# Kernel optimization log

Hardware: AMD Instinct MI355X
Metric: run time of the kernel (lower is better)

Reference implementation:

```python
import jax, jax.numpy as jnp
import numpy as np
from jax import lax

N, D, H, E = 8192, 1024, 4096, 8


def setup_inputs() -> dict:
    key = jax.random.key(0)
    ks = jax.random.split(key, 4)
    return {
        "x": jax.random.normal(ks[0], (N, D), dtype=jnp.float32),
        "wg": jax.random.normal(ks[1], (D, E), dtype=jnp.float32) * 0.001,
        "fc1_w": jax.random.normal(ks[2], (E, D, H), dtype=jnp.float32) * 0.001,
        "fc1_b": jnp.zeros((E, 1, H), dtype=jnp.float32),
        "fc2_w": jax.random.normal(ks[3], (E, H, D), dtype=jnp.float32) * 0.001,
        "fc2_b": jnp.zeros((E, 1, D), dtype=jnp.float32),
        "k": 2,
    }


def reference(x, wg, fc1_w, fc1_b, fc2_w, fc2_b, k):
    n, d = x.shape
    e = wg.shape[1]
    cap = (k * n) // e  # expert capacity (capacity factor 1.0)

    # --- gate ---
    scores = jax.nn.softmax(x @ wg, axis=-1)          # [N,E]
    topv, topi = lax.top_k(scores, k)                 # [N,k]

    # --- top-k routing: position of each (token, slot) within its expert buffer ---
    masks = jax.nn.one_hot(topi, e, dtype=jnp.int32)  # [N,k,E]
    # slot-major priority: all slot-0 assignments before slot-1
    m = jnp.transpose(masks, (1, 0, 2)).reshape(k * n, e)
    pos_flat = jnp.cumsum(m, axis=0) - m              # position before own assignment
    pos = jnp.sum(pos_flat * m, axis=1).reshape(k, n).T   # [N,k]
    valid = pos < cap                                  # capacity overflow -> dropped

    # --- load-balance aux loss (top-1 fraction * mean gate prob) ---
    me = scores.mean(axis=0)                           # [E]
    ce = masks[:, 0, :].astype(scores.dtype).mean(axis=0)
    l_aux = e * jnp.sum(me * ce)

    # --- encode (dispatch): scatter tokens into [E, C, D] buffers ---
    w = valid.astype(x.dtype)                          # [N,k]
    flat_idx = topi * cap + jnp.where(valid, pos, 0)   # [N,k]
    contrib = (x[:, None, :] * w[:, :, None]).reshape(-1, d)
    dispatched = jnp.zeros((e * cap, d), x.dtype).at[flat_idx.reshape(-1)].add(contrib)
    dispatched = dispatched.reshape(e, cap, d)

    # --- batched expert FFN (all-to-all is identity on one device) ---
    h = jax.nn.relu(jnp.einsum('ecd,edh->ech', dispatched, fc1_w) + fc1_b)
    y = jnp.einsum('ech,ehd->ecd', h, fc2_w) + fc2_b   # [E,C,D]

    # --- decode (combine): gather back and weight by gate scores ---
    gathered = y.reshape(e * cap, d)[flat_idx]         # [N,k,D]
    output = jnp.einsum('nk,nkd->nd', topv * w, gathered)
    return output, l_aux
```

## Files before the change

### kernel.cpp

```cpp
#include <hip/hip_runtime.h>
#include <hip/hip_bf16.h>
#include <stdint.h>

#define N_TOK 8192
#define DMODEL 1024
#define HDIM 4096
#define NEXP 8
#define CAP 2048
#define GATE_BLOCKS (N_TOK / 4)

typedef float floatx4 __attribute__((ext_vector_type(4)));
typedef int int32x4_t __attribute__((ext_vector_type(4)));
typedef int int32x8_t __attribute__((ext_vector_type(8)));

static __device__ __forceinline__ void async_copy16(const void* g, void* l) {
  __builtin_amdgcn_global_load_lds(
      (const __attribute__((address_space(1))) void*)g,
      (__attribute__((address_space(3))) void*)l, 16, 0, 0);
}

static __device__ __forceinline__ unsigned int pk4_fp8(float a, float b, float c, float d) {
  int r = __builtin_amdgcn_cvt_pk_fp8_f32(a, b, 0, 0);
  r = __builtin_amdgcn_cvt_pk_fp8_f32(c, d, r, 1);
  return (unsigned int)r;
}

static __device__ __forceinline__ unsigned short f2bf(float f) {
  union { float f; uint32_t u; } v; v.f = f;
  uint32_t r = (v.u + 0x7FFFu + ((v.u >> 16) & 1u)) >> 16;
  return (unsigned short)r;
}

static __device__ __forceinline__ float bf2f(unsigned short u) {
  union { float f; uint32_t u32; } v; v.u32 = ((uint32_t)u) << 16;
  return v.f;
}

__global__ __launch_bounds__(256) void gate_kernel(
    const float* __restrict__ x, const float* __restrict__ wg,
    float* __restrict__ topv, int* __restrict__ topi,
    float* __restrict__ me_part, int* __restrict__ ce_part) {
  __shared__ float sm_p[4][NEXP];
  __shared__ int sm_i0[4];
  int wave = threadIdx.x >> 6;
  int lane = threadIdx.x & 63;
  int n = blockIdx.x * 4 + wave;
  float acc[NEXP];
#pragma unroll
  for (int e = 0; e < NEXP; e++) acc[e] = 0.f;
  const float* xr = x + (size_t)n * DMODEL;
#pragma unroll 4
  for (int i = 0; i < DMODEL / 64; i++) {
    int idx = lane + 64 * i;
    float xv = xr[idx];
    const float4* wr = (const float4*)(wg + (size_t)idx * NEXP);
    float4 w0 = wr[0], w1 = wr[1];
    acc[0] += xv * w0.x; acc[1] += xv * w0.y;
    acc[2] += xv * w0.z; acc[3] += xv * w0.w;
    acc[4] += xv * w1.x; acc[5] += xv * w1.y;
    acc[6] += xv * w1.z; acc[7] += xv * w1.w;
  }
#pragma unroll
  for (int e = 0; e < NEXP; e++) {
    float v = acc[e];
#pragma unroll
    for (int off = 32; off > 0; off >>= 1) v += __shfl_down(v, off, 64);
    acc[e] = v;
  }
  if (lane == 0) {
    float mx = acc[0];
#pragma unroll
    for (int e = 1; e < NEXP; e++) mx = fmaxf(mx, acc[e]);
    float p[NEXP]; float s = 0.f;
#pragma unroll
    for (int e = 0; e < NEXP; e++) { p[e] = expf(acc[e] - mx); s += p[e]; }
    float inv = 1.f / s;
#pragma unroll
    for (int e = 0; e < NEXP; e++) p[e] *= inv;
    int i0 = 0; float v0 = p[0];
#pragma unroll
    for (int e = 1; e < NEXP; e++) if (p[e] > v0) { v0 = p[e]; i0 = e; }
    int i1 = -1; float v1 = -1.f;
#pragma unroll
    for (int e = 0; e < NEXP; e++) {
      if (e == i0) continue;
      if (p[e] > v1) { v1 = p[e]; i1 = e; }
    }
    topv[n * 2] = v0; topv[n * 2 + 1] = v1;
    topi[n * 2] = i0; topi[n * 2 + 1] = i1;
#pragma unroll
    for (int e = 0; e < NEXP; e++) sm_p[wave][e] = p[e];
    sm_i0[wave] = i0;
  }
  __syncthreads();
  if (threadIdx.x < NEXP) {
    int e = threadIdx.x;
    float pm = 0.f; int cc = 0;
#pragma unroll
    for (int w = 0; w < 4; w++) {
      pm += sm_p[w][e];
      cc += (sm_i0[w] == e) ? 1 : 0;
    }
    me_part[blockIdx.x * NEXP + e] = pm;
    ce_part[blockIdx.x * NEXP + e] = cc;
  }
}

__global__ __launch_bounds__(1024) void scan_kernel(
    const int* __restrict__ topi, const float* __restrict__ topv,
    int* __restrict__ flat_idx, float* __restrict__ cw) {
  __shared__ int hist[16][NEXP];
  __shared__ int base[NEXP];
  int tid = threadIdx.x;
  int w = tid >> 6, lane = tid & 63;
  if (tid < NEXP) base[tid] = 0;
  int vals[16];
#pragma unroll
  for (int c = 0; c < 16; c++) {
    int j = c * 1024 + tid;
    vals[c] = topi[(size_t)(j & 8191) * 2 + (j >> 13)];
  }
  __syncthreads();
  for (int c = 0; c < 16; c++) {
    int j = c * 1024 + tid;
    int slot = j >> 13;
    int n = j & 8191;
    int e = vals[c];
    int rank = 0;
#pragma unroll
    for (int ee = 0; ee < NEXP; ee++) {
      unsigned long long m = __ballot(e == ee);
      if (e == ee) rank = __popcll(m & ((1ull << lane) - 1ull));
      if (lane == ee) hist[w][ee] = __popcll(m);
    }
    __syncthreads();
    if (tid < NEXP) {
      int run = base[tid];
#pragma unroll
      for (int ww = 0; ww < 16; ww++) {
        int t = hist[ww][tid];
        hist[ww][tid] = run;
        run += t;
      }
      base[tid] = run;
    }
    __syncthreads();
    int pos = hist[w][e] + rank;
    bool valid = pos < CAP;
    flat_idx[n * 2 + slot] = e * CAP + (valid ? pos : 0);
    cw[n * 2 + slot] = valid ? topv[n * 2 + slot] : 0.f;
    __syncthreads();
  }
}

__global__ __launch_bounds__(256) void transpose_cvt_fp8(
    const float* __restrict__ in, unsigned char* __restrict__ out,
    int R, int C) {
  __shared__ float tile[32][129];
  const float* inp = in + (size_t)blockIdx.z * R * C;
  unsigned char* outp = out + (size_t)blockIdx.z * R * C;
  int c0 = blockIdx.x * 32, r0 = blockIdx.y * 128;
  int t = threadIdx.x;
#pragma unroll
  for (int p = 0; p < 4; p++) {
    int r = p * 32 + (t >> 3);
    int c4 = (t & 7) * 4;
    float4 v = *(const float4*)(inp + (size_t)(r0 + r) * C + c0 + c4);
    tile[c4 + 0][r] = v.x; tile[c4 + 1][r] = v.y;
    tile[c4 + 2][r] = v.z; tile[c4 + 3][r] = v.w;
  }
  __syncthreads();
  int c = t >> 3, r16 = (t & 7) * 16;
  unsigned int w[4];
#pragma unroll
  for (int j = 0; j < 4; j++) {
    float a = tile[c][r16 + j * 4 + 0] * 512.f;
    float b = tile[c][r16 + j * 4 + 1] * 512.f;
    float cc2 = tile[c][r16 + j * 4 + 2] * 512.f;
    float d = tile[c][r16 + j * 4 + 3] * 512.f;
    w[j] = pk4_fp8(a, b, cc2, d);
  }
  uint4 o; o.x = w[0]; o.y = w[1]; o.z = w[2]; o.w = w[3];
  *(uint4*)(outp + (size_t)(c0 + c) * R + r0 + r16) = o;
}

__global__ __launch_bounds__(64) void dispatch_kernel(
    const float* __restrict__ x, const int* __restrict__ flat_idx,
    const float* __restrict__ cw, unsigned char* __restrict__ disp) {
  int a = blockIdx.x;
  if (cw[a] == 0.f) return;
  int n = a >> 1;
  int f = flat_idx[a];
  int lane = threadIdx.x;
  const float4* xr = (const float4*)(x + (size_t)n * DMODEL);
  unsigned int* dr = (unsigned int*)(disp + (size_t)f * DMODEL);
#pragma unroll
  for (int i = 0; i < 4; i++) {
    float4 v = xr[lane + 64 * i];
    dr[lane + 64 * i] = pk4_fp8(v.x, v.y, v.z, v.w);
  }
}

template <int K_DIM, bool RELU, int OUT_MODE>
__global__ __launch_bounds__(256) void gemm_fp8_kernel(
    const unsigned char* __restrict__ A, const unsigned char* __restrict__ BT,
    const float* __restrict__ bias, void* __restrict__ Cout, int M, int Ncols,
    float inv_scale, float out_mult) {
  constexpr int BK = 128;
  constexpr int NSTAGE = K_DIM / BK;
  __shared__ unsigned char As[128 * BK];
  __shared__ unsigned char Bs[128 * BK];
  int e = blockIdx.z;
  int tn = blockIdx.x, tm = blockIdx.y;
  const unsigned char* Ae = A + (size_t)e * M * K_DIM + (size_t)tm * 128 * K_DIM;
  const unsigned char* Be = BT + (size_t)e * Ncols * K_DIM + (size_t)tn * 128 * K_DIM;
  int wv = threadIdx.x >> 6, l = threadIdx.x & 63;
  int wm = wv >> 1, wn = wv & 1;
  int l15 = l & 15, quad = l >> 4;
  int rbase = wv * 8 + (l >> 3);
  int cg = (l & 7) ^ ((l >> 3) & 7);
  floatx4 acc[4][4] = {};

#define STAGE_LOADS(k0)                                                        \
  {                                                                            \
    _Pragma("unroll") for (int i = 0; i < 4; i++) {                            \
      int r = rbase + i * 32;                                                  \
      async_copy16(Ae + (size_t)r * K_DIM + (k0) + cg * 16,                    \
                   As + i * 4096 + wv * 1024);                                 \
      async_copy16(Be + (size_t)r * K_DIM + (k0) + cg * 16,                    \
                   Bs + i * 4096 + wv * 1024);                                 \
    }                                                                          \
  }

  STAGE_LOADS(0);
#pragma unroll
  for (int s = 0; s < NSTAGE; s++) {
    __syncthreads();
    int32x8_t af[4], bf[4];
#pragma unroll
    for (int mi = 0; mi < 4; mi++) {
      int m = wm * 64 + mi * 16 + l15;
      int x0 = (quad * 2) ^ (m & 7), x1 = (quad * 2 + 1) ^ (m & 7);
      int32x4_t lo = *(const int32x4_t*)(As + m * 128 + x0 * 16);
      int32x4_t hi = *(const int32x4_t*)(As + m * 128 + x1 * 16);
      af[mi] = __builtin_shufflevector(lo, hi, 0, 1, 2, 3, 4, 5, 6, 7);
    }
#pragma unroll
    for (int ni = 0; ni < 4; ni++) {
      int m = wn * 64 + ni * 16 + l15;
      int x0 = (quad * 2) ^ (m & 7), x1 = (quad * 2 + 1) ^ (m & 7);
      int32x4_t lo = *(const int32x4_t*)(Bs + m * 128 + x0 * 16);
      int32x4_t hi = *(const int32x4_t*)(Bs + m * 128 + x1 * 16);
      bf[ni] = __builtin_shufflevector(lo, hi, 0, 1, 2, 3, 4, 5, 6, 7);
    }
    __syncthreads();
    if (s + 1 < NSTAGE) STAGE_LOADS((s + 1) * BK);
#pragma unroll
    for (int mi = 0; mi < 4; mi++)
#pragma unroll
      for (int ni = 0; ni < 4; ni++)
        acc[mi][ni] = __builtin_amdgcn_mfma_scale_f32_16x16x128_f8f6f4(
            af[mi], bf[ni], acc[mi][ni], 0, 0, 0, 0x7F7F7F7F, 0, 0x7F7F7F7F);
  }
#undef STAGE_LOADS

  int row_base = tm * 128 + wm * 64;
  int col_base = tn * 128 + wn * 64;
  const float* be = bias + (size_t)e * Ncols;
#pragma unroll
  for (int ni = 0; ni < 4; ni++) {
    int col = col_base + ni * 16 + l15;
    float bv = be[col];
#pragma unroll
    for (int mi = 0; mi < 4; mi++) {
#pragma unroll
      for (int r = 0; r < 4; r++) {
        int row = row_base + mi * 16 + quad * 4 + r;
        float v = acc[mi][ni][r] * inv_scale + bv;
        if (RELU) v = fmaxf(v, 0.f);
        size_t idx = (size_t)e * M * Ncols + (size_t)row * Ncols + col;
        if (OUT_MODE == 1) {
          float s = fminf(fmaxf(v * out_mult, -440.f), 440.f);
          unsigned int b8 = (unsigned int)__builtin_amdgcn_cvt_pk_fp8_f32(s, s, 0, 0) & 0xFF;
          ((unsigned char*)Cout)[idx] = (unsigned char)b8;
        } else if (OUT_MODE == 2) {
          ((unsigned short*)Cout)[idx] = f2bf(v);
        } else {
          ((float*)Cout)[idx] = v;
        }
      }
    }
  }
}

__global__ __launch_bounds__(256) void combine_kernel(
    const unsigned short* __restrict__ y, const int* __restrict__ flat_idx,
    const float* __restrict__ cw, float* __restrict__ out) {
  int n = blockIdx.x;
  float w0 = cw[n * 2], w1 = cw[n * 2 + 1];
  int f0 = flat_idx[n * 2], f1 = flat_idx[n * 2 + 1];
  const ushort2* y0 = (const ushort2*)(y + (size_t)f0 * DMODEL);
  const ushort2* y1 = (const ushort2*)(y + (size_t)f1 * DMODEL);
  float2* o = (float2*)(out + (size_t)n * DMODEL);
  int t = threadIdx.x;
#pragma unroll
  for (int i = 0; i < 2; i++) {
    int j = t + i * 256;
    ushort2 a = y0[j], b = y1[j];
    float2 r;
    r.x = w0 * bf2f(a.x) + w1 * bf2f(b.x);
    r.y = w0 * bf2f(a.y) + w1 * bf2f(b.y);
    o[j] = r;
  }
}

__global__ __launch_bounds__(256) void laux_kernel(
    const float* __restrict__ me_part, const int* __restrict__ ce_part,
    float* __restrict__ out_laux) {
  __shared__ float sme[NEXP][33];
  __shared__ float sce[NEXP][33];
  int tid = threadIdx.x;
  int e = tid >> 5;
  int c = tid & 31;
  float pm = 0.f, cc = 0.f;
  for (int b = c; b < GATE_BLOCKS; b += 32) {
    pm += me_part[b * NEXP + e];
    cc += (float)ce_part[b * NEXP + e];
  }
  sme[e][c] = pm;
  sce[e][c] = cc;
  __syncthreads();
  if (tid < NEXP) {
    float tm = 0.f, tc = 0.f;
#pragma unroll
    for (int i = 0; i < 32; i++) { tm += sme[tid][i]; tc += sce[tid][i]; }
    sme[tid][32] = tm;
    sce[tid][32] = tc;
  }
  __syncthreads();
  if (tid == 0) {
    float s = 0.f;
#pragma unroll
    for (int ee = 0; ee < NEXP; ee++)
      s += (sme[ee][32] / (float)N_TOK) * (sce[ee][32] / (float)N_TOK);
    *out_laux = (float)NEXP * s;
  }
}

extern "C" void kernel_launch(void* const* d_in, const int* in_sizes, int n_in,
                              void* d_out, int out_size, void* d_ws,
                              size_t ws_size, hipStream_t stream) {
  (void)in_sizes; (void)n_in; (void)out_size; (void)ws_size;
  const float* x     = (const float*)d_in[0];
  const float* wg    = (const float*)d_in[1];
  const float* fc1_w = (const float*)d_in[2];
  const float* fc1_b = (const float*)d_in[3];
  const float* fc2_w = (const float*)d_in[4];
  const float* fc2_b = (const float*)d_in[5];
  float* out = (float*)d_out;

  char* ws = (char*)d_ws;
  size_t o = 0;
  unsigned char* fc1t = (unsigned char*)(ws + o); o += (size_t)NEXP * DMODEL * HDIM;
  unsigned char* fc2t = (unsigned char*)(ws + o); o += (size_t)NEXP * DMODEL * HDIM;
  unsigned char* disp = (unsigned char*)(ws + o); o += (size_t)NEXP * CAP * DMODEL;
  unsigned char* hbuf = (unsigned char*)(ws + o); o += (size_t)NEXP * CAP * HDIM;
  unsigned short* ybuf = (unsigned short*)(ws + o); o += (size_t)NEXP * CAP * DMODEL * 2;
  float* topv = (float*)(ws + o); o += (size_t)N_TOK * 2 * 4;
  int* topi   = (int*)(ws + o);   o += (size_t)N_TOK * 2 * 4;
  int* flat   = (int*)(ws + o);   o += (size_t)N_TOK * 2 * 4;
  float* cw   = (float*)(ws + o); o += (size_t)N_TOK * 2 * 4;
  float* mep  = (float*)(ws + o); o += (size_t)GATE_BLOCKS * NEXP * 4;
  int* cep    = (int*)(ws + o);   o += (size_t)GATE_BLOCKS * NEXP * 4;


  gate_kernel<<<GATE_BLOCKS, 256, 0, stream>>>(x, wg, topv, topi, mep, cep);
  scan_kernel<<<1, 1024, 0, stream>>>(topi, topv, flat, cw);
  transpose_cvt_fp8<<<dim3(HDIM / 32, DMODEL / 128, NEXP), 256, 0, stream>>>(fc1_w, fc1t, DMODEL, HDIM);
  transpose_cvt_fp8<<<dim3(DMODEL / 32, HDIM / 128, NEXP), 256, 0, stream>>>(fc2_w, fc2t, HDIM, DMODEL);
  dispatch_kernel<<<N_TOK * 2, 64, 0, stream>>>(x, flat, cw, disp);
  gemm_fp8_kernel<DMODEL, true, 1>
      <<<dim3(HDIM / 128, CAP / 128, NEXP), 256, 0, stream>>>(
          disp, fc1t, fc1_b, hbuf, CAP, HDIM, 1.f / 512.f, 16.f);
  gemm_fp8_kernel<HDIM, false, 2>
      <<<dim3(DMODEL / 128, CAP / 128, NEXP), 256, 0, stream>>>(
          hbuf, fc2t, fc2_b, ybuf, CAP, DMODEL, 1.f / 8192.f, 1.f);
  combine_kernel<<<N_TOK, 256, 0, stream>>>(ybuf, flat, cw, out);
  laux_kernel<<<1, 256, 0, stream>>>(mep, cep, out + (size_t)N_TOK * DMODEL);
}
```

Before: 610.7 us.

## Double-buffer LDS tiles in FP8 expert GEMM with explicit vmcnt waits

Splits the LDS A/B tiles into two buffers and prefetches two K stages ahead, so global-to-LDS async copies for stage s+2 overlap the MFMA work on stage s. The __syncthreads calls are replaced by explicit s_waitcnt vmcnt/lgkmcnt plus raw barriers, allowing one stage of loads to stay in flight. It also raises wave priority around the MFMA block. This doubles LDS use to 64KB per block, which may lower occupancy, and relies on the vmcnt(8) count matching the 8 async copies issued per stage.

```diff
diff --git a/kernel.cpp b/kernel.cpp
--- a/kernel.cpp
+++ b/kernel.cpp
@@ -208,8 +208,9 @@
     float inv_scale, float out_mult) {
   constexpr int BK = 128;
   constexpr int NSTAGE = K_DIM / BK;
-  __shared__ unsigned char As[128 * BK];
-  __shared__ unsigned char Bs[128 * BK];
+  static_assert(NSTAGE >= 2, "need >=2 K stages for the 2-deep pipeline");
+  __shared__ unsigned char As[2][128 * BK];
+  __shared__ unsigned char Bs[2][128 * BK];
   int e = blockIdx.z;
   int tn = blockIdx.x, tm = blockIdx.y;
   const unsigned char* Ae = A + (size_t)e * M * K_DIM + (size_t)tm * 128 * K_DIM;
@@ -221,46 +222,55 @@
   int cg = (l & 7) ^ ((l >> 3) & 7);
   floatx4 acc[4][4] = {};
 
-#define STAGE_LOADS(k0)                                                        \
+#define STAGE_LOADS(k0, buf)                                                   \
   {                                                                            \
     _Pragma("unroll") for (int i = 0; i < 4; i++) {                            \
       int r = rbase + i * 32;                                                  \
       async_copy16(Ae + (size_t)r * K_DIM + (k0) + cg * 16,                    \
-                   As + i * 4096 + wv * 1024);                                 \
+                   &As[buf][i * 4096 + wv * 1024]);                            \
       async_copy16(Be + (size_t)r * K_DIM + (k0) + cg * 16,                    \
-                   Bs + i * 4096 + wv * 1024);                                 \
+                   &Bs[buf][i * 4096 + wv * 1024]);                            \
     }                                                                          \
   }
 
-  STAGE_LOADS(0);
+  STAGE_LOADS(0, 0);
+  STAGE_LOADS(BK, 1);
 #pragma unroll
   for (int s = 0; s < NSTAGE; s++) {
-    __syncthreads();
+    const int cur = s & 1;
+    if (s + 1 < NSTAGE)
+      asm volatile("s_waitcnt vmcnt(8)" ::: "memory");
+    else
+      asm volatile("s_waitcnt vmcnt(0)" ::: "memory");
+    __builtin_amdgcn_s_barrier();
     int32x8_t af[4], bf[4];
 #pragma unroll
     for (int mi = 0; mi < 4; mi++) {
       int m = wm * 64 + mi * 16 + l15;
       int x0 = (quad * 2) ^ (m & 7), x1 = (quad * 2 + 1) ^ (m & 7);
-      int32x4_t lo = *(const int32x4_t*)(As + m * 128 + x0 * 16);
-      int32x4_t hi = *(const int32x4_t*)(As + m * 128 + x1 * 16);
+      int32x4_t lo = *(const int32x4_t*)(&As[cur][m * 128 + x0 * 16]);
+      int32x4_t hi = *(const int32x4_t*)(&As[cur][m * 128 + x1 * 16]);
       af[mi] = __builtin_shufflevector(lo, hi, 0, 1, 2, 3, 4, 5, 6, 7);
     }
 #pragma unroll
     for (int ni = 0; ni < 4; ni++) {
       int m = wn * 64 + ni * 16 + l15;
       int x0 = (quad * 2) ^ (m & 7), x1 = (quad * 2 + 1) ^ (m & 7);
-      int32x4_t lo = *(const int32x4_t*)(Bs + m * 128 + x0 * 16);
-      int32x4_t hi = *(const int32x4_t*)(Bs + m * 128 + x1 * 16);
+      int32x4_t lo = *(const int32x4_t*)(&Bs[cur][m * 128 + x0 * 16]);
+      int32x4_t hi = *(const int32x4_t*)(&Bs[cur][m * 128 + x1 * 16]);
       bf[ni] = __builtin_shufflevector(lo, hi, 0, 1, 2, 3, 4, 5, 6, 7);
     }
-    __syncthreads();
-    if (s + 1 < NSTAGE) STAGE_LOADS((s + 1) * BK);
+    asm volatile("s_waitcnt lgkmcnt(0)" ::: "memory");
+    __builtin_amdgcn_s_barrier();
+    if (s + 2 < NSTAGE) STAGE_LOADS((s + 2) * BK, cur);
+    __builtin_amdgcn_s_setprio(1);
 #pragma unroll
     for (int mi = 0; mi < 4; mi++)
 #pragma unroll
       for (int ni = 0; ni < 4; ni++)
         acc[mi][ni] = __builtin_amdgcn_mfma_scale_f32_16x16x128_f8f6f4(
             af[mi], bf[ni], acc[mi][ni], 0, 0, 0, 0x7F7F7F7F, 0, 0x7F7F7F7F);
+    __builtin_amdgcn_s_setprio(0);
   }
 #undef STAGE_LOADS
 
```

Result: faster. 588.9 us (-3.6%).
